# Performance work log

Measured on AMD Instinct MI355X. Metric: run time of the kernel, lower is better.

Reference implementation:

```python
import jax, jax.numpy as jnp
import numpy as np

B, CIN, COUT, H, W, K = 8, 128, 128, 32, 32, 3
FULL = K * K  # 9 kernel taps
EPS = 1e-7


def inv3(b):
    # batched closed-form 3x3 inverse via adjugate, matching torch inverse3 (det + eps)
    b00, b01, b02 = b[:, 0, 0], b[:, 0, 1], b[:, 0, 2]
    b10, b11, b12 = b[:, 1, 0], b[:, 1, 1], b[:, 1, 2]
    b20, b21, b22 = b[:, 2, 0], b[:, 2, 1], b[:, 2, 2]
    det = (b00 * (b11 * b22 - b12 * b21)
           - b01 * (b10 * b22 - b12 * b20)
           + b02 * (b10 * b21 - b11 * b20)) + EPS
    c = jnp.stack([
        b11 * b22 - b12 * b21, b02 * b21 - b01 * b22, b01 * b12 - b02 * b11,
        b12 * b20 - b10 * b22, b00 * b22 - b02 * b20, b02 * b10 - b00 * b12,
        b10 * b21 - b11 * b20, b01 * b20 - b00 * b21, b00 * b11 - b01 * b10,
    ], axis=-1)  # (N, 9)
    return (c / det[:, None]).reshape(-1, 3, 3)


def cayley_kernels(kernel):
    # kernel: (16,) params -> per-tap 3x3 Cayley matrices G (9,3,3)
    # torch loop: num = i except i==8 -> kern//2 = 1; i==4 -> identity; a = b = kernel[2*num], c = kernel[2*num+1]
    nums = jnp.array([0, 1, 2, 3, 0, 5, 6, 7, 1])
    a = kernel[2 * nums]
    c = kernel[2 * nums + 1]
    o = jnp.ones_like(a)
    # first[i] = [[1,-a,-a],[a,1,-c],[a,c,1]]
    F = jnp.stack([o, -a, -a, a, o, -c, a, c, o], axis=-1).reshape(FULL, 3, 3)
    eye = jnp.eye(3, dtype=kernel.dtype)
    F = F.at[4].set(eye)
    S = 2.0 * eye - F  # second = sign-flipped off-diagonals; S[4] = eye
    return jnp.matmul(inv3(F), S)  # (9,3,3)


def setup_inputs() -> dict:
    key = jax.random.key(0)
    k1, k2 = jax.random.split(key)
    x = jax.random.normal(k1, (B, CIN, H, W, 3, 3), dtype=jnp.float32)
    g = jax.random.uniform(k2, ((FULL - 1) * 2 + CIN * COUT,), dtype=jnp.float32) - 0.5
    return {"x": x, "g": g}


def reference(x, g):
    kernel = g[:(FULL - 1) * 2]
    G = cayley_kernels(kernel)  # (9,3,3), tap t = kh*3 + kw
    # y[b,c,h,w,t,i,j] = (G_t @ X @ G_t^T)[i,j]
    y = jnp.einsum('tip,bchwpq,tjq->bcthwij', G, x, G)
    Ho, Wo = H + K - 1, W + K - 1
    # fold: matrix-element index (mi,mj) acts as the 3x3 spatial offset (layout aliasing in torch code);
    # kernel tap t stays a channel sub-index -> folded[b,c,t, h+mi, w+mj] += y[b,c,t,h,w,mi,mj]
    folded = jnp.zeros((B, CIN, FULL, Ho, Wo), dtype=y.dtype)
    for mi in range(3):
        for mj in range(3):
            folded = folded.at[:, :, :, mi:mi + H, mj:mj + W].add(y[..., mi, mj])
    # channel mixing with squared (nonneg) weights
    c_mat = (g[(FULL - 1) * 2:] ** 2).reshape(CIN, COUT)
    mixed = jnp.einsum('bcthw,co->bothw', folded, c_mat)  # (B,COUT,9,Ho,Wo)
    out = jnp.transpose(mixed, (0, 1, 3, 4, 2)).reshape(B, COUT, Ho, Wo, 3, 3)
    result = 0.5 * (out + jnp.swapaxes(out, -1, -2))
    return result
```

## Files before the change

### kernel.cpp

```cpp
#include <hip/hip_runtime.h>

#define NB    8
#define CIN   128
#define COUT  128
#define HH    32
#define WW    32
#define HO    34
#define WO    34
#define SSP   (HO*WO)
#define SPAD  1160
#define UU    6
#define NS    (SPAD*UU)
#define NT    48
#define EPSC  1e-7f

typedef __attribute__((ext_vector_type(8))) short bf16x8;
typedef __attribute__((ext_vector_type(4))) float f32x4;

__device__ __forceinline__ ushort f2b(float f) {
  uint u = __float_as_uint(f);
  uint r = (u + 0x7fffu + ((u >> 16) & 1u)) >> 16;
  return (ushort)r;
}

__global__ void prep_kernel(const float* __restrict__ g,
                            float* __restrict__ M,
                            ushort* __restrict__ wT) {
  if (blockIdx.x == 0) {
    __shared__ float Gs[81];
    int t = threadIdx.x;
    if (t < 9) {
      const int nums[9] = {0,1,2,3,0,5,6,7,1};
      float a = g[2*nums[t]];
      float c = g[2*nums[t]+1];
      float F[9], S2[9];
      if (t == 4) {
        F[0]=1;F[1]=0;F[2]=0;F[3]=0;F[4]=1;F[5]=0;F[6]=0;F[7]=0;F[8]=1;
        S2[0]=1;S2[1]=0;S2[2]=0;S2[3]=0;S2[4]=1;S2[5]=0;S2[6]=0;S2[7]=0;S2[8]=1;
      } else {
        F[0]=1.f; F[1]=-a;  F[2]=-a;
        F[3]=a;   F[4]=1.f; F[5]=-c;
        F[6]=a;   F[7]=c;   F[8]=1.f;
        S2[0]=1.f;  S2[1]=a;   S2[2]=a;
        S2[3]=-a;   S2[4]=1.f; S2[5]=c;
        S2[6]=-a;   S2[7]=-c;  S2[8]=1.f;
      }
      float det = F[0]*(F[4]*F[8]-F[5]*F[7]) - F[1]*(F[3]*F[8]-F[5]*F[6])
                + F[2]*(F[3]*F[7]-F[4]*F[6]) + EPSC;
      float inv[9];
      inv[0] = (F[4]*F[8]-F[5]*F[7]);
      inv[1] = (F[2]*F[7]-F[1]*F[8]);
      inv[2] = (F[1]*F[5]-F[2]*F[4]);
      inv[3] = (F[5]*F[6]-F[3]*F[8]);
      inv[4] = (F[0]*F[8]-F[2]*F[6]);
      inv[5] = (F[2]*F[3]-F[0]*F[5]);
      inv[6] = (F[3]*F[7]-F[4]*F[6]);
      inv[7] = (F[1]*F[6]-F[0]*F[7]);
      inv[8] = (F[0]*F[4]-F[1]*F[3]);
      float rd = 1.0f/det;
      #pragma unroll
      for (int i = 0; i < 9; ++i) inv[i] *= rd;
      #pragma unroll
      for (int i = 0; i < 3; ++i)
        #pragma unroll
        for (int j = 0; j < 3; ++j)
          Gs[t*9+i*3+j] = inv[i*3+0]*S2[0*3+j] + inv[i*3+1]*S2[1*3+j] + inv[i*3+2]*S2[2*3+j];
    }
    __syncthreads();
    if (t < 6) {
      const int T1[6] = {0,1,2,4,5,8};
      const int T2[6] = {0,3,6,4,7,8};
      int t1 = T1[t], t2 = T2[t];
      for (int co = 0; co < 9; ++co) {
        int i = co/3, j = co%3;
        for (int k = 0; k < 9; ++k) {
          int p = k/3, q = k%3;
          M[t*81 + co*9 + k] =
            0.5f*(Gs[t1*9+i*3+p]*Gs[t1*9+j*3+q] + Gs[t2*9+i*3+p]*Gs[t2*9+j*3+q]);
        }
      }
    }
  } else {
    int idx = (int)(blockIdx.x-1)*256 + threadIdx.x;
    int o = idx >> 7, c = idx & 127;
    float w = g[16 + c*128 + o];
    wT[idx] = f2b(w*w);
  }
}

__global__ __launch_bounds__(512) void fold_kernel(const float* __restrict__ x,
                                                   const float* __restrict__ M,
                                                   ushort* __restrict__ folded) {
  __shared__ float4 XsA[1024];
  __shared__ float4 XsB[1024];
  __shared__ float  XsC[1024];
  int tid = threadIdx.x;
  const float* xb = x + (size_t)blockIdx.x * (HH*WW*9);

  #pragma unroll
  for (int kk = 0; kk < 2; ++kk) {
    int px = tid + kk*512;
    const float* p = xb + px*9;
    XsA[px] = make_float4(p[0],p[1],p[2],p[3]);
    XsB[px] = make_float4(p[4],p[5],p[6],p[7]);
    XsC[px] = p[8];
  }
  __syncthreads();

  float acc[3][6];
  #pragma unroll
  for (int r = 0; r < 3; ++r)
    #pragma unroll
    for (int u = 0; u < 6; ++u) acc[r][u] = 0.f;

  int hoA[3], woA[3];
  #pragma unroll
  for (int r = 0; r < 3; ++r) {
    int idx = tid + r*512;
    int hh = (int)((uint)idx / 34u);
    hoA[r] = hh;
    woA[r] = idx - 34*hh;
  }

  for (int tap = 0; tap < 9; ++tap) {
    int ti = tap / 3;
    int tj = tap - 3*ti;
    const float* Mt = M + tap*9;
    float m[6][9];
    #pragma unroll
    for (int u = 0; u < 6; ++u)
      #pragma unroll
      for (int k = 0; k < 9; ++k)
        m[u][k] = Mt[u*81 + k];

    #pragma unroll
    for (int r = 0; r < 3; ++r) {
      int idx = tid + r*512;
      if (r < 2 || idx < SSP) {
        int hh = hoA[r] - ti;
        int wj = woA[r] - tj;
        bool ok = ((uint)hh < 32u) && ((uint)wj < 32u);
        int px = hh*32 + wj;
        px = min(max(px, 0), 1023);
        float4 a = XsA[px];
        float4 b = XsB[px];
        float  c = XsC[px];
        float msk = ok ? 1.f : 0.f;
        float v[9] = {a.x,a.y,a.z,a.w,b.x,b.y,b.z,b.w,c};
        #pragma unroll
        for (int u = 0; u < 6; ++u) {
          float d = m[u][0]*v[0];
          #pragma unroll
          for (int k = 1; k < 9; ++k) d = fmaf(m[u][k], v[k], d);
          acc[r][u] = fmaf(msk, d, acc[r][u]);
        }
      }
    }
  }

  uint* outp = (uint*)folded + (size_t)blockIdx.x * (NS/2);
  #pragma unroll
  for (int r = 0; r < 3; ++r) {
    int idx = tid + r*512;
    if (idx < SPAD) {
      uint p0 = (uint)f2b(acc[r][0]) | ((uint)f2b(acc[r][1]) << 16);
      uint p1 = (uint)f2b(acc[r][2]) | ((uint)f2b(acc[r][3]) << 16);
      uint p2 = (uint)f2b(acc[r][4]) | ((uint)f2b(acc[r][5]) << 16);
      outp[idx*3+0] = p0;
      outp[idx*3+1] = p1;
      outp[idx*3+2] = p2;
    }
  }
}

__global__ __launch_bounds__(192) void gemm_kernel(const ushort* __restrict__ wT,
                                                   const ushort* __restrict__ folded,
                                                   float* __restrict__ out) {
  __shared__ __align__(16) char smem[128*52*4];
  ushort* ldsB = (ushort*)smem;
  float*  ldsC = (float*)smem;

  int tid  = threadIdx.x;
  int b    = blockIdx.y;
  int tile = blockIdx.x;
  int n0   = tile * NT;

  #pragma unroll
  for (int p = 0; p < 4; ++p) {
    int chunk = tid + p*192;
    int c  = chunk / 6;
    int nc = (chunk - 6*c) * 8;
    const ushort* src = folded + ((size_t)(b*CIN + c)*NS + n0 + nc);
    uint4 v = *(const uint4*)src;
    ushort e[8];
    e[0]=(ushort)(v.x & 0xffffu); e[1]=(ushort)(v.x >> 16);
    e[2]=(ushort)(v.y & 0xffffu); e[3]=(ushort)(v.y >> 16);
    e[4]=(ushort)(v.z & 0xffffu); e[5]=(ushort)(v.z >> 16);
    e[6]=(ushort)(v.w & 0xffffu); e[7]=(ushort)(v.w >> 16);
    #pragma unroll
    for (int j = 0; j < 8; ++j) {
      int nl  = nc + j;
      int ksw = c ^ (((nl >> 3) & 7) << 4);
      ldsB[nl*136 + ksw] = e[j];
    }
  }
  __syncthreads();

  int wave = tid >> 6, lane = tid & 63;
  int l15 = lane & 15, lhi = lane >> 4;
  int nl = wave*16 + l15;
  int sw = ((nl >> 3) & 7) << 4;

  f32x4 acc[8];
  #pragma unroll
  for (int i = 0; i < 8; ++i) acc[i] = (f32x4){0.f,0.f,0.f,0.f};

  const ushort* wrow = wT + l15*128;
  #pragma unroll
  for (int k0 = 0; k0 < 128; k0 += 32) {
    int kk = k0 + lhi*8;
    bf16x8 bfrag = *(const bf16x8*)&ldsB[nl*136 + (kk ^ sw)];
    #pragma unroll
    for (int mf = 0; mf < 8; ++mf) {
      bf16x8 afrag = *(const bf16x8*)(wrow + mf*16*128 + kk);
      acc[mf] = __builtin_amdgcn_mfma_f32_16x16x32_bf16(afrag, bfrag, acc[mf], 0, 0, 0);
    }
  }

  __syncthreads();
  #pragma unroll
  for (int mf = 0; mf < 8; ++mf)
    #pragma unroll
    for (int r = 0; r < 4; ++r) {
      int o = mf*16 + lhi*4 + r;
      ldsC[o*52 + nl] = acc[mf][r];
    }
  __syncthreads();

  int s0 = tile * 8;
  const int umap[9] = {0,1,2,1,3,4,2,4,5};
  #pragma unroll
  for (int r = 0; r < 6; ++r) {
    int pair = tid + r*192;
    if (pair < 1024) {
      int o  = pair >> 3;
      int sl = pair & 7;
      int s  = s0 + sl;
      if (s < SSP) {
        float v[6];
        #pragma unroll
        for (int u = 0; u < 6; ++u) v[u] = ldsC[o*52 + sl*6 + u];
        size_t base = ((size_t)(b*COUT + o)*SSP + s)*9;
        #pragma unroll
        for (int t = 0; t < 9; ++t) out[base + t] = v[umap[t]];
      }
    }
  }
}

extern "C" void kernel_launch(void* const* d_in, const int* in_sizes, int n_in,
                              void* d_out, int out_size, void* d_ws, size_t ws_size,
                              hipStream_t stream) {
  const float* x = (const float*)d_in[0];
  const float* g = (const float*)d_in[1];
  float* out = (float*)d_out;

  float*  M      = (float*)d_ws;
  ushort* wT     = (ushort*)((char*)d_ws + 4096);
  ushort* folded = (ushort*)((char*)d_ws + 4096 + 32768);

  prep_kernel<<<65, 256, 0, stream>>>(g, M, wT);
  fold_kernel<<<NB*CIN, 512, 0, stream>>>(x, M, folded);
  gemm_kernel<<<dim3(NS/NT, NB), 192, 0, stream>>>(wT, folded, out);
}
```

Before: 129.5 us.

## Use fp16 packed dot products in fold and split gemm across six waves

The fold kernel now stores input tiles in LDS as packed fp16 and computes the per-tap 9-term contractions with fdot2 instructions, reading fp16-packed coefficients prepared by prep_kernel. Out-of-range pixels read a zero sentinel entry instead of being masked. The gemm kernel moves from 192 to 384 threads, splitting the output channels across two wave groups and preloading A fragments into registers. This cuts LDS traffic and ALU work, and raises parallelism in the GEMM, at the cost of fp16 rounding of inputs and coefficients and higher register pressure.

```diff
diff --git a/kernel.cpp b/kernel.cpp
--- a/kernel.cpp
+++ b/kernel.cpp
@@ -16,15 +16,20 @@
 
 typedef __attribute__((ext_vector_type(8))) short bf16x8;
 typedef __attribute__((ext_vector_type(4))) float f32x4;
+typedef __attribute__((ext_vector_type(2))) _Float16 h2;
 
 __device__ __forceinline__ ushort f2b(float f) {
   uint u = __float_as_uint(f);
   uint r = (u + 0x7fffu + ((u >> 16) & 1u)) >> 16;
   return (ushort)r;
 }
+__device__ __forceinline__ uint pkh(float a, float b) {
+  return __builtin_bit_cast(uint, __builtin_amdgcn_cvt_pkrtz(a, b));
+}
+__device__ __forceinline__ h2 ash2(uint u) { return __builtin_bit_cast(h2, u); }
 
 __global__ void prep_kernel(const float* __restrict__ g,
-                            float* __restrict__ M,
+                            uint* __restrict__ Mh,
                             ushort* __restrict__ wT) {
   if (blockIdx.x == 0) {
     __shared__ float Gs[81];
@@ -71,13 +76,16 @@
       const int T1[6] = {0,1,2,4,5,8};
       const int T2[6] = {0,3,6,4,7,8};
       int t1 = T1[t], t2 = T2[t];
-      for (int co = 0; co < 9; ++co) {
-        int i = co/3, j = co%3;
+      for (int tap = 0; tap < 9; ++tap) {
+        int i = tap/3, j = tap%3;
+        float m[10];
         for (int k = 0; k < 9; ++k) {
           int p = k/3, q = k%3;
-          M[t*81 + co*9 + k] =
-            0.5f*(Gs[t1*9+i*3+p]*Gs[t1*9+j*3+q] + Gs[t2*9+i*3+p]*Gs[t2*9+j*3+q]);
+          m[k] = 0.5f*(Gs[t1*9+i*3+p]*Gs[t1*9+j*3+q] + Gs[t2*9+i*3+p]*Gs[t2*9+j*3+q]);
         }
+        m[9] = 0.f;
+        for (int d = 0; d < 5; ++d)
+          Mh[(tap*6 + t)*5 + d] = pkh(m[2*d], m[2*d+1]);
       }
     }
   } else {
@@ -88,12 +96,12 @@
   }
 }
 
-__global__ __launch_bounds__(512) void fold_kernel(const float* __restrict__ x,
-                                                   const float* __restrict__ M,
-                                                   ushort* __restrict__ folded) {
-  __shared__ float4 XsA[1024];
-  __shared__ float4 XsB[1024];
-  __shared__ float  XsC[1024];
+__global__ __launch_bounds__(512, 6) void fold_kernel(const float* __restrict__ x,
+                                                      const uint* __restrict__ Mh,
+                                                      ushort* __restrict__ folded) {
+  __shared__ uint2 XsA[1025];
+  __shared__ uint2 XsB[1025];
+  __shared__ uint  XsC[1025];
   int tid = threadIdx.x;
   const float* xb = x + (size_t)blockIdx.x * (HH*WW*9);
 
@@ -101,9 +109,14 @@
   for (int kk = 0; kk < 2; ++kk) {
     int px = tid + kk*512;
     const float* p = xb + px*9;
-    XsA[px] = make_float4(p[0],p[1],p[2],p[3]);
-    XsB[px] = make_float4(p[4],p[5],p[6],p[7]);
-    XsC[px] = p[8];
+    XsA[px] = make_uint2(pkh(p[0],p[1]), pkh(p[2],p[3]));
+    XsB[px] = make_uint2(pkh(p[4],p[5]), pkh(p[6],p[7]));
+    XsC[px] = pkh(p[8], 0.f);
+  }
+  if (tid == 0) {
+    XsA[1024] = make_uint2(0u,0u);
+    XsB[1024] = make_uint2(0u,0u);
+    XsC[1024] = 0u;
   }
   __syncthreads();
 
@@ -122,40 +135,36 @@
     woA[r] = idx - 34*hh;
   }
 
+  int ti = 0, tj = 0;
   for (int tap = 0; tap < 9; ++tap) {
-    int ti = tap / 3;
-    int tj = tap - 3*ti;
-    const float* Mt = M + tap*9;
-    float m[6][9];
-    #pragma unroll
-    for (int u = 0; u < 6; ++u)
-      #pragma unroll
-      for (int k = 0; k < 9; ++k)
-        m[u][k] = Mt[u*81 + k];
+    const uint* C = Mh + tap*30;
+    uint cu[30];
+    #pragma unroll
+    for (int j = 0; j < 30; ++j) cu[j] = C[j];
 
     #pragma unroll
     for (int r = 0; r < 3; ++r) {
-      int idx = tid + r*512;
-      if (r < 2 || idx < SSP) {
-        int hh = hoA[r] - ti;
-        int wj = woA[r] - tj;
-        bool ok = ((uint)hh < 32u) && ((uint)wj < 32u);
-        int px = hh*32 + wj;
-        px = min(max(px, 0), 1023);
-        float4 a = XsA[px];
-        float4 b = XsB[px];
-        float  c = XsC[px];
-        float msk = ok ? 1.f : 0.f;
-        float v[9] = {a.x,a.y,a.z,a.w,b.x,b.y,b.z,b.w,c};
-        #pragma unroll
-        for (int u = 0; u < 6; ++u) {
-          float d = m[u][0]*v[0];
-          #pragma unroll
-          for (int k = 1; k < 9; ++k) d = fmaf(m[u][k], v[k], d);
-          acc[r][u] = fmaf(msk, d, acc[r][u]);
-        }
-      }
-    }
+      int hh = hoA[r] - ti;
+      int wj = woA[r] - tj;
+      bool ok = ((uint)hh < 32u) && ((uint)wj < 32u);
+      int px = ok ? (hh*32 + wj) : 1024;
+      uint2 a = XsA[px];
+      uint2 b = XsB[px];
+      uint  c = XsC[px];
+      h2 v0 = ash2(a.x), v1 = ash2(a.y), v2 = ash2(b.x), v3 = ash2(b.y), v4 = ash2(c);
+      #pragma unroll
+      for (int u = 0; u < 6; ++u) {
+        float d = acc[r][u];
+        d = __builtin_amdgcn_fdot2(ash2(cu[u*5+0]), v0, d, false);
+        d = __builtin_amdgcn_fdot2(ash2(cu[u*5+1]), v1, d, false);
+        d = __builtin_amdgcn_fdot2(ash2(cu[u*5+2]), v2, d, false);
+        d = __builtin_amdgcn_fdot2(ash2(cu[u*5+3]), v3, d, false);
+        d = __builtin_amdgcn_fdot2(ash2(cu[u*5+4]), v4, d, false);
+        acc[r][u] = d;
+      }
+    }
+
+    if (++tj == 3) { tj = 0; ++ti; }
   }
 
   uint* outp = (uint*)folded + (size_t)blockIdx.x * (NS/2);
@@ -173,7 +182,7 @@
   }
 }
 
-__global__ __launch_bounds__(192) void gemm_kernel(const ushort* __restrict__ wT,
+__global__ __launch_bounds__(384) void gemm_kernel(const ushort* __restrict__ wT,
                                                    const ushort* __restrict__ folded,
                                                    float* __restrict__ out) {
   __shared__ __align__(16) char smem[128*52*4];
@@ -185,9 +194,26 @@
   int tile = blockIdx.x;
   int n0   = tile * NT;
 
-  #pragma unroll
-  for (int p = 0; p < 4; ++p) {
-    int chunk = tid + p*192;
+  int wave = tid >> 6, lane = tid & 63;
+  int l15 = lane & 15, lhi = lane >> 4;
+  int ng = wave % 3;
+  int mh = wave / 3;
+  int nl = ng*16 + l15;
+  int sw = ((nl >> 3) & 7) << 4;
+
+  bf16x8 af[4][4];
+  {
+    const ushort* arow = wT + (mh*64 + l15)*128 + lhi*8;
+    #pragma unroll
+    for (int mf = 0; mf < 4; ++mf)
+      #pragma unroll
+      for (int k0 = 0; k0 < 4; ++k0)
+        af[mf][k0] = *(const bf16x8*)(arow + mf*16*128 + k0*32);
+  }
+
+  #pragma unroll
+  for (int p = 0; p < 2; ++p) {
+    int chunk = tid + p*384;
     int c  = chunk / 6;
     int nc = (chunk - 6*c) * 8;
     const ushort* src = folded + ((size_t)(b*CIN + c)*NS + n0 + nc);
@@ -199,40 +225,32 @@
     e[6]=(ushort)(v.w & 0xffffu); e[7]=(ushort)(v.w >> 16);
     #pragma unroll
     for (int j = 0; j < 8; ++j) {
-      int nl  = nc + j;
-      int ksw = c ^ (((nl >> 3) & 7) << 4);
-      ldsB[nl*136 + ksw] = e[j];
-    }
-  }
-  __syncthreads();
-
-  int wave = tid >> 6, lane = tid & 63;
-  int l15 = lane & 15, lhi = lane >> 4;
-  int nl = wave*16 + l15;
-  int sw = ((nl >> 3) & 7) << 4;
-
-  f32x4 acc[8];
-  #pragma unroll
-  for (int i = 0; i < 8; ++i) acc[i] = (f32x4){0.f,0.f,0.f,0.f};
-
-  const ushort* wrow = wT + l15*128;
-  #pragma unroll
-  for (int k0 = 0; k0 < 128; k0 += 32) {
-    int kk = k0 + lhi*8;
+      int nj  = nc + j;
+      int ksw = c ^ (((nj >> 3) & 7) << 4);
+      ldsB[nj*136 + ksw] = e[j];
+    }
+  }
+  __syncthreads();
+
+  f32x4 acc[4];
+  #pragma unroll
+  for (int i = 0; i < 4; ++i) acc[i] = (f32x4){0.f,0.f,0.f,0.f};
+
+  #pragma unroll
+  for (int k0 = 0; k0 < 4; ++k0) {
+    int kk = k0*32 + lhi*8;
     bf16x8 bfrag = *(const bf16x8*)&ldsB[nl*136 + (kk ^ sw)];
     #pragma unroll
-    for (int mf = 0; mf < 8; ++mf) {
-      bf16x8 afrag = *(const bf16x8*)(wrow + mf*16*128 + kk);
-      acc[mf] = __builtin_amdgcn_mfma_f32_16x16x32_bf16(afrag, bfrag, acc[mf], 0, 0, 0);
-    }
-  }
-
-  __syncthreads();
-  #pragma unroll
-  for (int mf = 0; mf < 8; ++mf)
+    for (int mf = 0; mf < 4; ++mf)
+      acc[mf] = __builtin_amdgcn_mfma_f32_16x16x32_bf16(af[mf][k0], bfrag, acc[mf], 0, 0, 0);
+  }
+
+  __syncthreads();
+  #pragma unroll
+  for (int mf = 0; mf < 4; ++mf)
     #pragma unroll
     for (int r = 0; r < 4; ++r) {
-      int o = mf*16 + lhi*4 + r;
+      int o = mh*64 + mf*16 + lhi*4 + r;
       ldsC[o*52 + nl] = acc[mf][r];
     }
   __syncthreads();
@@ -240,8 +258,8 @@
   int s0 = tile * 8;
   const int umap[9] = {0,1,2,1,3,4,2,4,5};
   #pragma unroll
-  for (int r = 0; r < 6; ++r) {
-    int pair = tid + r*192;
+  for (int r = 0; r < 3; ++r) {
+    int pair = tid + r*384;
     if (pair < 1024) {
       int o  = pair >> 3;
       int sl = pair & 7;
@@ -265,11 +283,11 @@
   const float* g = (const float*)d_in[1];
   float* out = (float*)d_out;
 
-  float*  M      = (float*)d_ws;
+  uint*   Mh     = (uint*)d_ws;
   ushort* wT     = (ushort*)((char*)d_ws + 4096);
   ushort* folded = (ushort*)((char*)d_ws + 4096 + 32768);
 
-  prep_kernel<<<65, 256, 0, stream>>>(g, M, wT);
-  fold_kernel<<<NB*CIN, 512, 0, stream>>>(x, M, folded);
-  gemm_kernel<<<dim3(NS/NT, NB), 192, 0, stream>>>(wT, folded, out);
-}
+  prep_kernel<<<65, 256, 0, stream>>>(g, Mh, wT);
+  fold_kernel<<<NB*CIN, 512, 0, stream>>>(x, Mh, folded);
+  gemm_kernel<<<dim3(NS/NT, NB), 384, 0, stream>>>(wT, folded, out);
+}
```

New measurement: 129.0 us. Within noise of the previous version (-0.4%).
